# Optimization experiments

Measured on AMD Instinct MI355X. Metric: run time of the kernel, lower is better.

The kernel has to match this reference:

```python
import jax, jax.numpy as jnp
import numpy as np

NEG_SLOPE = 0.2
EPS = 1e-16


def gat_conv(x, edge_index, W, att_src, att_dst, bias, heads, out_ch, concat):
    """PyG-style GATConv (eval mode, add_self_loops=True)."""
    N = x.shape[0]
    h = (x @ W).reshape(N, heads, out_ch)              # [N,H,C]
    loop = jnp.arange(N, dtype=edge_index.dtype)
    src = jnp.concatenate([edge_index[0], loop])       # [E+N]
    dst = jnp.concatenate([edge_index[1], loop])
    a_src = jnp.sum(h * att_src, axis=-1)              # [N,H]
    a_dst = jnp.sum(h * att_dst, axis=-1)
    e = jax.nn.leaky_relu(a_src[src] + a_dst[dst], NEG_SLOPE)  # [E+N,H]
    # segment softmax over destination nodes
    m = jax.ops.segment_max(e, dst, num_segments=N)
    e = jnp.exp(e - m[dst])
    s = jax.ops.segment_sum(e, dst, num_segments=N)
    alpha = e / (s[dst] + EPS)                         # [E+N,H]
    msg = h[src] * alpha[..., None]                    # [E+N,H,C]
    out = jax.ops.segment_sum(msg, dst, num_segments=N)  # [N,H,C]
    out = out.reshape(N, heads * out_ch) if concat else out.mean(axis=1)
    return out + bias


def setup_inputs() -> dict:
    key = jax.random.key(0)
    ks = jax.random.split(key, 11)
    N, F, E = 100000, 128, 1600000
    H1, C1 = 4, 16
    H2, C2 = 1, 16
    return {
        "x": jax.random.normal(ks[0], (N, F), dtype=jnp.float32),
        "edge_index": jax.random.randint(ks[1], (2, E), 0, N, dtype=jnp.int64) if jax.config.jax_enable_x64 else jax.random.randint(ks[1], (2, E), 0, N).astype(jnp.int32),
        "W1": jax.random.normal(ks[2], (F, H1 * C1), dtype=jnp.float32) * 0.1,
        "att_src1": jax.random.normal(ks[3], (H1, C1), dtype=jnp.float32) * 0.1,
        "att_dst1": jax.random.normal(ks[4], (H1, C1), dtype=jnp.float32) * 0.1,
        "bias1": jax.random.normal(ks[5], (H1 * C1,), dtype=jnp.float32) * 0.1,
        "W2": jax.random.normal(ks[6], (H1 * C1, H2 * C2), dtype=jnp.float32) * 0.1,
        "att_src2": jax.random.normal(ks[7], (H2, C2), dtype=jnp.float32) * 0.1,
        "att_dst2": jax.random.normal(ks[8], (H2, C2), dtype=jnp.float32) * 0.1,
        "bias2": jax.random.normal(ks[9], (C2,), dtype=jnp.float32) * 0.1,
    }


def reference(x, edge_index, W1, att_src1, att_dst1, bias1, W2, att_src2, att_dst2, bias2):
    # dropout is identity in eval mode
    h = gat_conv(x, edge_index, W1, att_src1, att_dst1, bias1, heads=4, out_ch=16, concat=True)
    h = jax.nn.elu(h)
    h = gat_conv(h, edge_index, W2, att_src2, att_dst2, bias2, heads=1, out_ch=16, concat=False)
    return jax.nn.log_softmax(h, axis=1)
```

## Files before the change

### kernel.cpp

```cpp
#include <hip/hip_runtime.h>
#include <hip/hip_fp16.h>
#include <hip/hip_bf16.h>
#include <math.h>


#define LRELU(v) ((v) > 0.f ? (v) : 0.2f * (v))
#define BSH 8
#define BCAP 5120
#define CHK 8192
#define CAP1 64
#define CAP2 64

typedef __attribute__((ext_vector_type(8))) short short8;
typedef __attribute__((ext_vector_type(8))) _Float16 half8;
typedef __attribute__((ext_vector_type(4))) float float4v;

static __device__ __forceinline__ short f2bf(float f) {
    __hip_bfloat16 b = __float2bfloat16(f);
    return *reinterpret_cast<short*>(&b);
}

__global__ __launch_bounds__(256) void k_scatter(const int* __restrict__ ei, int* __restrict__ cursor,
                                                 int* __restrict__ stage, int E, int NBK) {
    __shared__ int hist[512];
    __shared__ int cnt2[512];
    __shared__ int base[512];
    int tid = threadIdx.x;
    int e0 = blockIdx.x * CHK;
    int nedge = E - e0; if (nedge > CHK) nedge = CHK;

    for (int i = tid; i < 512; i += 256) { hist[i] = 0; cnt2[i] = 0; }
    __syncthreads();
    for (int j = tid; j < nedge; j += 256) {
        int d = ei[E + e0 + j];
        atomicAdd(&hist[d >> BSH], 1);
    }
    __syncthreads();
    for (int b = tid; b < NBK; b += 256) {
        int c = hist[b];
        if (c > 0) base[b] = b * BCAP + atomicAdd(&cursor[b], c);
    }
    __syncthreads();
    for (int j = tid; j < nedge; j += 256) {
        int s = ei[e0 + j];
        int d = ei[E + e0 + j];
        int b = d >> BSH;
        int r = atomicAdd(&cnt2[b], 1);
        stage[base[b] + r] = s | ((d & ((1 << BSH) - 1)) << 17);
    }
}

__global__ __launch_bounds__(256) void k_build(const int* __restrict__ stage,
                                               const int* __restrict__ cursor,
                                               int* __restrict__ row_start,
                                               int* __restrict__ csr,
                                               const float* __restrict__ W1,
                                               const float* __restrict__ att_src,
                                               const float* __restrict__ att_dst,
                                               float* __restrict__ Wc,
                                               const float* __restrict__ W2,
                                               const float* __restrict__ att_src2,
                                               const float* __restrict__ att_dst2,
                                               float* __restrict__ Wc2,
                                               int NBK, int E, int N) {
    __shared__ int cnt[256];
    __shared__ int lb[256];
    __shared__ int cur[256];
    __shared__ int sA[256];
    int b = blockIdx.x, tid = threadIdx.x;
    int nodes0 = b << BSH;
    int nnodes = N - nodes0; if (nnodes > 256) nnodes = 256;
    int partial = 0;
    for (int i = tid; i < b; i += 256) partial += cursor[i];
    sA[tid] = partial;
    __syncthreads();
    for (int off = 128; off >= 1; off >>= 1) {
        if (tid < off) sA[tid] += sA[tid + off];
        __syncthreads();
    }
    int ebase = sA[0];
    int ecnt = cursor[b];
    __syncthreads();
    if (b == 0) {
        if (tid == 0) row_start[N] = E + N;
        for (int i = tid; i < 16 * 128; i += 256) {
            int col = i >> 7, k = i & 127;
            float v = 0.f;
            if (col < 8) {
                int h = col & 3;
                const float* att = (col < 4) ? att_src : att_dst;
                #pragma unroll
                for (int c = 0; c < 16; c++) v += W1[k * 64 + h * 16 + c] * att[h * 16 + c];
            }
            Wc[i] = v;
        }
        for (int i = tid; i < 128; i += 256) {
            int col = i >> 6, k = i & 63;
            const float* att = col ? att_dst2 : att_src2;
            float v = 0.f;
            #pragma unroll
            for (int c = 0; c < 16; c++) v += W2[k * 16 + c] * att[c];
            Wc2[i] = v;
        }
    }
    const int* sbk = stage + b * BCAP;
    cnt[tid] = (tid < nnodes) ? 1 : 0;
    __syncthreads();
    for (int e = tid; e < ecnt; e += 256) {
        int l = (sbk[e] >> 17) & 255;
        atomicAdd(&cnt[l], 1);
    }
    __syncthreads();
    int myc = cnt[tid];
    sA[tid] = myc;
    __syncthreads();
    for (int off = 1; off < 256; off <<= 1) {
        int r = sA[tid] + ((tid >= off) ? sA[tid - off] : 0);
        __syncthreads();
        sA[tid] = r;
        __syncthreads();
    }
    int gb = ebase + nodes0;
    lb[tid] = sA[tid] - myc;
    cur[tid] = 1;
    __syncthreads();
    if (tid < nnodes) {
        row_start[nodes0 + tid] = gb + lb[tid];
        csr[gb + lb[tid]] = nodes0 + tid;
    }
    __syncthreads();
    for (int e = tid; e < ecnt; e += 256) {
        int v = sbk[e];
        int l = (v >> 17) & 255;
        int src = v & 0x1FFFF;
        int r = atomicAdd(&cur[l], 1);
        csr[gb + lb[l] + r] = src;
    }
}

__global__ __launch_bounds__(256) void k_gemm1(const float* __restrict__ x,
                                               const float* __restrict__ W1,
                                               const float* __restrict__ Wc,
                                               __half* __restrict__ h1, float* __restrict__ a_src,
                                               float* __restrict__ a_dst, int N) {
    __shared__ short wt[80 * 136];
    int tid = threadIdx.x;
    for (int i = tid; i < 128 * 64; i += 256) {
        int k = i >> 6, c = i & 63;
        wt[c * 136 + k] = f2bf(W1[i]);
    }
    for (int i = tid; i < 16 * 128; i += 256) {
        int col = i >> 7, k = i & 127;
        wt[(64 + col) * 136 + k] = f2bf(Wc[i]);
    }
    __syncthreads();
    int wave = tid >> 6, lane = tid & 63;
    int m = lane & 15, q = lane >> 4;
    int nbase = blockIdx.x * 64 + wave * 16;
    int anode = nbase + m;
    bool rowok = anode < N;
    const float* xrow = x + (size_t)(rowok ? anode : 0) * 128 + q * 8;

    float4v acc[5];
    #pragma unroll
    for (int ct = 0; ct < 5; ct++)
        #pragma unroll
        for (int r = 0; r < 4; r++) acc[ct][r] = 0.f;

    #pragma unroll
    for (int kc = 0; kc < 4; kc++) {
        float4 u0 = make_float4(0.f, 0.f, 0.f, 0.f), u1 = u0;
        if (rowok) {
            u0 = *(const float4*)(xrow + kc * 32);
            u1 = *(const float4*)(xrow + kc * 32 + 4);
        }
        short8 af;
        af[0] = f2bf(u0.x); af[1] = f2bf(u0.y); af[2] = f2bf(u0.z); af[3] = f2bf(u0.w);
        af[4] = f2bf(u1.x); af[5] = f2bf(u1.y); af[6] = f2bf(u1.z); af[7] = f2bf(u1.w);
        #pragma unroll
        for (int ct = 0; ct < 5; ct++) {
            short8 bf = *(const short8*)&wt[(ct * 16 + m) * 136 + kc * 32 + q * 8];
            acc[ct] = __builtin_amdgcn_mfma_f32_16x16x32_bf16(af, bf, acc[ct], 0, 0, 0);
        }
    }
    #pragma unroll
    for (int ct = 0; ct < 4; ct++) {
        #pragma unroll
        for (int r = 0; r < 4; r++) {
            int n = nbase + q * 4 + r;
            if (n < N) h1[(size_t)n * 64 + ct * 16 + m] = __float2half(acc[ct][r]);
        }
    }
    #pragma unroll
    for (int r = 0; r < 4; r++) {
        int n = nbase + q * 4 + r;
        if (n < N) {
            float v = acc[4][r];
            if (m < 4) a_src[n * 4 + m] = v;
            else if (m < 8) a_dst[n * 4 + (m - 4)] = v;
        }
    }
}

__global__ __launch_bounds__(256) void k_agg1(const int* __restrict__ row_start,
                                              const int* __restrict__ csr_src,
                                              const float* __restrict__ a_src,
                                              const float* __restrict__ a_dst,
                                              const __half* __restrict__ h1,
                                              const float* __restrict__ bias,
                                              __half* __restrict__ out1, int N) {
    __shared__ int   sidx[16][CAP1];
    __shared__ float sval[16][CAP1 * 4];
    int tid = threadIdx.x;
    int wave = tid >> 6, lane = tid & 63;
    int quad = lane >> 4, l16 = lane & 15;
    int slot = wave * 4 + quad;
    int node = blockIdx.x * 16 + slot;
    if (node >= N) return;
    int row = row_start[node];
    int deg = row_start[node + 1] - row;
    float4 ad = ((const float4*)a_dst)[node];
    float s0 = 0.f, s1 = 0.f, s2 = 0.f, s3 = 0.f;
    for (int j = l16; j < deg; j += 16) {
        int s = csr_src[row + j];
        float4 as = ((const float4*)a_src)[s];
        float e0 = __expf(LRELU(as.x + ad.x));
        float e1 = __expf(LRELU(as.y + ad.y));
        float e2 = __expf(LRELU(as.z + ad.z));
        float e3 = __expf(LRELU(as.w + ad.w));
        if (j < CAP1) {
            sidx[slot][j] = s;
            *(float4*)&sval[slot][j * 4] = make_float4(e0, e1, e2, e3);
        }
        s0 += e0; s1 += e1; s2 += e2; s3 += e3;
    }
    #pragma unroll
    for (int m = 1; m < 16; m <<= 1) {
        s0 += __shfl_xor(s0, m, 64);
        s1 += __shfl_xor(s1, m, 64);
        s2 += __shfl_xor(s2, m, 64);
        s3 += __shfl_xor(s3, m, 64);
    }
    int myh = l16 >> 2;
    float ssv = myh == 0 ? s0 : myh == 1 ? s1 : myh == 2 ? s2 : s3;
    float adm = myh == 0 ? ad.x : myh == 1 ? ad.y : myh == 2 ? ad.z : ad.w;
    float iv = 1.f / (ssv + 1e-16f);
    float A0 = 0.f, A1 = 0.f, A2 = 0.f, A3 = 0.f;
    float B0 = 0.f, B1 = 0.f, B2 = 0.f, B3 = 0.f;
    int dc = deg < CAP1 ? deg : CAP1;
    int j = 0;
    for (; j + 8 <= dc; j += 8) {
        int t[8]; float e[8]; float2 lo[8], hi[8];
        #pragma unroll
        for (int u = 0; u < 8; u++) {
            t[u] = sidx[slot][j + u];
            e[u] = sval[slot][(j + u) * 4 + myh];
        }
        #pragma unroll
        for (int u = 0; u < 8; u++) {
            union { float2 f; __half2 h[2]; } uu;
            uu.f = *(const float2*)&h1[(size_t)t[u] * 64 + l16 * 4];
            lo[u] = __half22float2(uu.h[0]);
            hi[u] = __half22float2(uu.h[1]);
        }
        #pragma unroll
        for (int u = 0; u < 8; u += 2) {
            A0 += e[u] * lo[u].x; A1 += e[u] * lo[u].y;
            A2 += e[u] * hi[u].x; A3 += e[u] * hi[u].y;
            B0 += e[u + 1] * lo[u + 1].x; B1 += e[u + 1] * lo[u + 1].y;
            B2 += e[u + 1] * hi[u + 1].x; B3 += e[u + 1] * hi[u + 1].y;
        }
    }
    for (; j < dc; j++) {
        int t = sidx[slot][j];
        float e = sval[slot][j * 4 + myh];
        union { float2 f; __half2 h[2]; } uu;
        uu.f = *(const float2*)&h1[(size_t)t * 64 + l16 * 4];
        float2 lo = __half22float2(uu.h[0]), hi = __half22float2(uu.h[1]);
        A0 += e * lo.x; A1 += e * lo.y; A2 += e * hi.x; A3 += e * hi.y;
    }
    for (; j < deg; j++) {
        int s = csr_src[row + j];
        float e = __expf(LRELU(a_src[s * 4 + myh] + adm));
        union { float2 f; __half2 h[2]; } uu;
        uu.f = *(const float2*)&h1[(size_t)s * 64 + l16 * 4];
        float2 lo = __half22float2(uu.h[0]), hi = __half22float2(uu.h[1]);
        A0 += e * lo.x; A1 += e * lo.y; A2 += e * hi.x; A3 += e * hi.y;
    }
    A0 += B0; A1 += B1; A2 += B2; A3 += B3;
    float4 bb = ((const float4*)bias)[l16];
    float o0 = A0 * iv + bb.x;
    float o1 = A1 * iv + bb.y;
    float o2 = A2 * iv + bb.z;
    float o3 = A3 * iv + bb.w;
    o0 = (o0 > 0.f) ? o0 : (__expf(o0) - 1.f);
    o1 = (o1 > 0.f) ? o1 : (__expf(o1) - 1.f);
    o2 = (o2 > 0.f) ? o2 : (__expf(o2) - 1.f);
    o3 = (o3 > 0.f) ? o3 : (__expf(o3) - 1.f);
    union { __half2 h2v[2]; float2 f2; } pk;
    pk.h2v[0] = __floats2half2_rn(o0, o1);
    pk.h2v[1] = __floats2half2_rn(o2, o3);
    *(float2*)&out1[(size_t)node * 64 + l16 * 4] = pk.f2;
}

__global__ __launch_bounds__(256) void k_gemm2(const __half* __restrict__ out1,
                                               const float* __restrict__ W2,
                                               const float* __restrict__ Wc2,
                                               __half* __restrict__ h2, float* __restrict__ a_src,
                                               float* __restrict__ a_dst, int N) {
    __shared__ _Float16 wt2[16][72];
    __shared__ _Float16 wtb[16][72];
    int tid = threadIdx.x;
    for (int i = tid; i < 16 * 64; i += 256) {
        int k = i >> 4, c = i & 15;
        wt2[c][k] = (_Float16)W2[i];
    }
    for (int i = tid; i < 16 * 64; i += 256) {
        int col = i >> 6, k = i & 63;
        wtb[col][k] = (col < 2) ? (_Float16)Wc2[col * 64 + k] : (_Float16)0.f;
    }
    __syncthreads();
    int wave = tid >> 6, lane = tid & 63;
    int m = lane & 15, q = lane >> 4;
    int nbase = blockIdx.x * 64 + wave * 16;
    int anode = nbase + m;
    bool ok = anode < N;
    const __half* arow = out1 + (size_t)(ok ? anode : 0) * 64 + q * 8;

    float4v c1 = {0.f, 0.f, 0.f, 0.f}, c2v = {0.f, 0.f, 0.f, 0.f};
    #pragma unroll
    for (int kc = 0; kc < 2; kc++) {
        half8 af = *(const half8*)(arow + kc * 32);
        half8 b1 = *(const half8*)&wt2[m][kc * 32 + q * 8];
        half8 b2 = *(const half8*)&wtb[m][kc * 32 + q * 8];
        c1  = __builtin_amdgcn_mfma_f32_16x16x32_f16(af, b1, c1, 0, 0, 0);
        c2v = __builtin_amdgcn_mfma_f32_16x16x32_f16(af, b2, c2v, 0, 0, 0);
    }
    #pragma unroll
    for (int r = 0; r < 4; r++) {
        int n = nbase + q * 4 + r;
        if (n < N) {
            h2[(size_t)n * 16 + m] = __float2half(c1[r]);
            if (m == 0) a_src[n] = c2v[r];
            else if (m == 1) a_dst[n] = c2v[r];
        }
    }
}

__global__ __launch_bounds__(256) void k_agg2(const int* __restrict__ row_start,
                                              const int* __restrict__ csr_src,
                                              const float* __restrict__ a_src,
                                              const float* __restrict__ a_dst,
                                              const __half* __restrict__ h2,
                                              const float* __restrict__ bias,
                                              float* __restrict__ out, int N) {
    __shared__ int   sidx[16][CAP2];
    __shared__ float sval[16][CAP2];
    int tid = threadIdx.x;
    int wave = tid >> 6, lane = tid & 63;
    int quad = lane >> 4, l16 = lane & 15;
    int slot = wave * 4 + quad;
    int node = blockIdx.x * 16 + slot;
    if (node >= N) return;
    int row = row_start[node];
    int deg = row_start[node + 1] - row;
    float ad = a_dst[node];
    float sh = 0.f;
    for (int j = l16; j < deg; j += 16) {
        int s = csr_src[row + j];
        float e = __expf(LRELU(a_src[s] + ad));
        if (j < CAP2) { sidx[slot][j] = s; sval[slot][j] = e; }
        sh += e;
    }
    #pragma unroll
    for (int m = 1; m < 16; m <<= 1) sh += __shfl_xor(sh, m, 64);
    float iv = 1.f / (sh + 1e-16f);
    int cg = l16 & 7, eg = l16 >> 3;
    float ax = 0.f, ay = 0.f, bx = 0.f, by = 0.f;
    int dc = deg < CAP2 ? deg : CAP2;
    int j = eg;
    for (; j + 6 < dc; j += 8) {
        int t0 = sidx[slot][j], t1 = sidx[slot][j + 2];
        int t2 = sidx[slot][j + 4], t3 = sidx[slot][j + 6];
        float e0 = sval[slot][j], e1 = sval[slot][j + 2];
        float e2 = sval[slot][j + 4], e3 = sval[slot][j + 6];
        float2 g0 = __half22float2(*(const __half2*)&h2[(size_t)t0 * 16 + cg * 2]);
        float2 g1 = __half22float2(*(const __half2*)&h2[(size_t)t1 * 16 + cg * 2]);
        float2 g2 = __half22float2(*(const __half2*)&h2[(size_t)t2 * 16 + cg * 2]);
        float2 g3 = __half22float2(*(const __half2*)&h2[(size_t)t3 * 16 + cg * 2]);
        ax += e0 * g0.x + e2 * g2.x; ay += e0 * g0.y + e2 * g2.y;
        bx += e1 * g1.x + e3 * g3.x; by += e1 * g1.y + e3 * g3.y;
    }
    for (; j < deg; j += 2) {
        int s; float e;
        if (j < dc) { s = sidx[slot][j]; e = sval[slot][j]; }
        else { s = csr_src[row + j]; e = __expf(LRELU(a_src[s] + ad)); }
        float2 g = __half22float2(*(const __half2*)&h2[(size_t)s * 16 + cg * 2]);
        ax += e * g.x; ay += e * g.y;
    }
    ax += bx; ay += by;
    ax += __shfl_xor(ax, 8, 64);
    ay += __shfl_xor(ay, 8, 64);
    float2 bb = ((const float2*)bias)[cg];
    float vx = ax * iv + bb.x;
    float vy = ay * iv + bb.y;
    float mx = fmaxf(vx, vy);
    #pragma unroll
    for (int m = 1; m < 8; m <<= 1) mx = fmaxf(mx, __shfl_xor(mx, m, 64));
    float se = __expf(vx - mx) + __expf(vy - mx);
    #pragma unroll
    for (int m = 1; m < 8; m <<= 1) se += __shfl_xor(se, m, 64);
    float ls = mx + __logf(se);
    if (eg == 0)
        ((float2*)out)[(size_t)node * 8 + cg] = make_float2(vx - ls, vy - ls);
}

extern "C" void kernel_launch(void* const* d_in, const int* in_sizes, int n_in,
                              void* d_out, int out_size, void* d_ws, size_t ws_size,
                              hipStream_t stream) {
    const float* x        = (const float*)d_in[0];
    const int*   ei       = (const int*)d_in[1];
    const float* W1       = (const float*)d_in[2];
    const float* att_src1 = (const float*)d_in[3];
    const float* att_dst1 = (const float*)d_in[4];
    const float* bias1    = (const float*)d_in[5];
    const float* W2       = (const float*)d_in[6];
    const float* att_src2 = (const float*)d_in[7];
    const float* att_dst2 = (const float*)d_in[8];
    const float* bias2    = (const float*)d_in[9];
    float* out = (float*)d_out;

    const int N = in_sizes[0] / 128;
    const int E = in_sizes[1] / 2;
    const int NBK = (N + 255) >> BSH;

    char* p = (char*)d_ws;
    auto alloc = [&](size_t bytes) -> void* {
        void* r = (void*)p;
        p += (bytes + 255) & ~(size_t)255;
        return r;
    };
    __half* h1     = (__half*)alloc((size_t)N * 64 * 2);
    __half* out1   = (__half*)alloc((size_t)N * 64 * 2);
    __half* h2     = (__half*)alloc((size_t)N * 16 * 2);
    float* a_src1  = (float*)alloc((size_t)N * 4 * 4);
    float* a_dst1  = (float*)alloc((size_t)N * 4 * 4);
    float* a_src2  = (float*)alloc((size_t)N * 4);
    float* a_dst2  = (float*)alloc((size_t)N * 4);
    float* Wc      = (float*)alloc(16 * 128 * 4);
    float* Wc2     = (float*)alloc(2 * 64 * 4);
    int*   row_st  = (int*)alloc((size_t)(N + 1) * 4);
    int*   csr     = (int*)alloc((size_t)(E + N) * 4);
    int*   stage   = (int*)alloc((size_t)NBK * BCAP * 4);
    int*   cursor  = (int*)alloc((size_t)NBK * 4);
    (void)ws_size; (void)n_in; (void)out_size;

    hipMemsetAsync(cursor, 0, (size_t)NBK * 4, stream);
    k_scatter<<<(E + CHK - 1) / CHK, 256, 0, stream>>>(ei, cursor, stage, E, NBK);
    k_build<<<NBK, 256, 0, stream>>>(stage, cursor, row_st, csr,
                                     W1, att_src1, att_dst1, Wc,
                                     W2, att_src2, att_dst2, Wc2, NBK, E, N);
    k_gemm1<<<(N + 63) / 64, 256, 0, stream>>>(x, W1, Wc, h1, a_src1, a_dst1, N);
    k_agg1<<<(N + 15) / 16, 256, 0, stream>>>(row_st, csr, a_src1, a_dst1, h1, bias1, out1, N);
    k_gemm2<<<(N + 63) / 64, 256, 0, stream>>>(out1, W2, Wc2, h2, a_src2, a_dst2, N);
    k_agg2<<<(N + 15) / 16, 256, 0, stream>>>(row_st, csr, a_src2, a_dst2, h2, bias2, out, N);
}
```

Before: 234.5 us.

## Remap aggregation kernels to four lanes per node with single-pass softmax

Both aggregation kernels now give each destination node 4 lanes (one per head in layer 1, one column quarter in layer 2) instead of 16. The two-phase scheme with LDS staging of edge indices and exp values is replaced by a single pass that accumulates the unnormalised weighted sum and the softmax denominator together, with wider 16-byte feature gathers. This removes shared memory, the cross-lane reductions and the second pass over edges, but each lane carries more registers and works through the degree loop serially, which may reduce memory-level parallelism per node.

```diff
diff --git a/kernel.cpp b/kernel.cpp
--- a/kernel.cpp
+++ b/kernel.cpp
@@ -8,11 +8,10 @@
 #define BSH 8
 #define BCAP 5120
 #define CHK 8192
-#define CAP1 64
-#define CAP2 64
 
 typedef __attribute__((ext_vector_type(8))) short short8;
 typedef __attribute__((ext_vector_type(8))) _Float16 half8;
+typedef __attribute__((ext_vector_type(4))) _Float16 half4;
 typedef __attribute__((ext_vector_type(4))) float float4v;
 
 static __device__ __forceinline__ short f2bf(float f) {
@@ -209,98 +208,82 @@
                                               const __half* __restrict__ h1,
                                               const float* __restrict__ bias,
                                               __half* __restrict__ out1, int N) {
-    __shared__ int   sidx[16][CAP1];
-    __shared__ float sval[16][CAP1 * 4];
     int tid = threadIdx.x;
     int wave = tid >> 6, lane = tid & 63;
-    int quad = lane >> 4, l16 = lane & 15;
-    int slot = wave * 4 + quad;
-    int node = blockIdx.x * 16 + slot;
+    int grp = lane >> 2, sub = lane & 3;
+    int node = blockIdx.x * 64 + wave * 16 + grp;
     if (node >= N) return;
     int row = row_start[node];
     int deg = row_start[node + 1] - row;
-    float4 ad = ((const float4*)a_dst)[node];
-    float s0 = 0.f, s1 = 0.f, s2 = 0.f, s3 = 0.f;
-    for (int j = l16; j < deg; j += 16) {
-        int s = csr_src[row + j];
-        float4 as = ((const float4*)a_src)[s];
-        float e0 = __expf(LRELU(as.x + ad.x));
-        float e1 = __expf(LRELU(as.y + ad.y));
-        float e2 = __expf(LRELU(as.z + ad.z));
-        float e3 = __expf(LRELU(as.w + ad.w));
-        if (j < CAP1) {
-            sidx[slot][j] = s;
-            *(float4*)&sval[slot][j * 4] = make_float4(e0, e1, e2, e3);
-        }
-        s0 += e0; s1 += e1; s2 += e2; s3 += e3;
-    }
-    #pragma unroll
-    for (int m = 1; m < 16; m <<= 1) {
-        s0 += __shfl_xor(s0, m, 64);
-        s1 += __shfl_xor(s1, m, 64);
-        s2 += __shfl_xor(s2, m, 64);
-        s3 += __shfl_xor(s3, m, 64);
-    }
-    int myh = l16 >> 2;
-    float ssv = myh == 0 ? s0 : myh == 1 ? s1 : myh == 2 ? s2 : s3;
-    float adm = myh == 0 ? ad.x : myh == 1 ? ad.y : myh == 2 ? ad.z : ad.w;
-    float iv = 1.f / (ssv + 1e-16f);
-    float A0 = 0.f, A1 = 0.f, A2 = 0.f, A3 = 0.f;
-    float B0 = 0.f, B1 = 0.f, B2 = 0.f, B3 = 0.f;
-    int dc = deg < CAP1 ? deg : CAP1;
+    float adm = a_dst[node * 4 + sub];
+    const _Float16* hb = (const _Float16*)h1 + sub * 16;
+    float A[16];
+    #pragma unroll
+    for (int c = 0; c < 16; c++) A[c] = 0.f;
+    float sh = 0.f;
     int j = 0;
-    for (; j + 8 <= dc; j += 8) {
-        int t[8]; float e[8]; float2 lo[8], hi[8];
+    for (; j + 4 <= deg; j += 4) {
+        int s0 = csr_src[row + j + 0];
+        int s1 = csr_src[row + j + 1];
+        int s2 = csr_src[row + j + 2];
+        int s3 = csr_src[row + j + 3];
+        float x0 = a_src[s0 * 4 + sub] + adm;
+        float x1 = a_src[s1 * 4 + sub] + adm;
+        float x2 = a_src[s2 * 4 + sub] + adm;
+        float x3 = a_src[s3 * 4 + sub] + adm;
+        half8 p0 = *(const half8*)(hb + (size_t)s0 * 64);
+        half8 q0 = *(const half8*)(hb + (size_t)s0 * 64 + 8);
+        half8 p1 = *(const half8*)(hb + (size_t)s1 * 64);
+        half8 q1 = *(const half8*)(hb + (size_t)s1 * 64 + 8);
+        half8 p2 = *(const half8*)(hb + (size_t)s2 * 64);
+        half8 q2 = *(const half8*)(hb + (size_t)s2 * 64 + 8);
+        half8 p3 = *(const half8*)(hb + (size_t)s3 * 64);
+        half8 q3 = *(const half8*)(hb + (size_t)s3 * 64 + 8);
+        float e0 = __expf(fmaxf(x0, 0.2f * x0));
+        float e1 = __expf(fmaxf(x1, 0.2f * x1));
+        float e2 = __expf(fmaxf(x2, 0.2f * x2));
+        float e3 = __expf(fmaxf(x3, 0.2f * x3));
+        sh += (e0 + e1) + (e2 + e3);
         #pragma unroll
-        for (int u = 0; u < 8; u++) {
-            t[u] = sidx[slot][j + u];
-            e[u] = sval[slot][(j + u) * 4 + myh];
-        }
-        #pragma unroll
-        for (int u = 0; u < 8; u++) {
-            union { float2 f; __half2 h[2]; } uu;
-            uu.f = *(const float2*)&h1[(size_t)t[u] * 64 + l16 * 4];
-            lo[u] = __half22float2(uu.h[0]);
-            hi[u] = __half22float2(uu.h[1]);
-        }
-        #pragma unroll
-        for (int u = 0; u < 8; u += 2) {
-            A0 += e[u] * lo[u].x; A1 += e[u] * lo[u].y;
-            A2 += e[u] * hi[u].x; A3 += e[u] * hi[u].y;
-            B0 += e[u + 1] * lo[u + 1].x; B1 += e[u + 1] * lo[u + 1].y;
-            B2 += e[u + 1] * hi[u + 1].x; B3 += e[u + 1] * hi[u + 1].y;
-        }
-    }
-    for (; j < dc; j++) {
-        int t = sidx[slot][j];
-        float e = sval[slot][j * 4 + myh];
-        union { float2 f; __half2 h[2]; } uu;
-        uu.f = *(const float2*)&h1[(size_t)t * 64 + l16 * 4];
-        float2 lo = __half22float2(uu.h[0]), hi = __half22float2(uu.h[1]);
-        A0 += e * lo.x; A1 += e * lo.y; A2 += e * hi.x; A3 += e * hi.y;
+        for (int c = 0; c < 8; c++) {
+            A[c]     += e0 * (float)p0[c] + e1 * (float)p1[c]
+                      + e2 * (float)p2[c] + e3 * (float)p3[c];
+            A[c + 8] += e0 * (float)q0[c] + e1 * (float)q1[c]
+                      + e2 * (float)q2[c] + e3 * (float)q3[c];
+        }
     }
     for (; j < deg; j++) {
         int s = csr_src[row + j];
-        float e = __expf(LRELU(a_src[s * 4 + myh] + adm));
-        union { float2 f; __half2 h[2]; } uu;
-        uu.f = *(const float2*)&h1[(size_t)s * 64 + l16 * 4];
-        float2 lo = __half22float2(uu.h[0]), hi = __half22float2(uu.h[1]);
-        A0 += e * lo.x; A1 += e * lo.y; A2 += e * hi.x; A3 += e * hi.y;
-    }
-    A0 += B0; A1 += B1; A2 += B2; A3 += B3;
-    float4 bb = ((const float4*)bias)[l16];
-    float o0 = A0 * iv + bb.x;
-    float o1 = A1 * iv + bb.y;
-    float o2 = A2 * iv + bb.z;
-    float o3 = A3 * iv + bb.w;
-    o0 = (o0 > 0.f) ? o0 : (__expf(o0) - 1.f);
-    o1 = (o1 > 0.f) ? o1 : (__expf(o1) - 1.f);
-    o2 = (o2 > 0.f) ? o2 : (__expf(o2) - 1.f);
-    o3 = (o3 > 0.f) ? o3 : (__expf(o3) - 1.f);
-    union { __half2 h2v[2]; float2 f2; } pk;
-    pk.h2v[0] = __floats2half2_rn(o0, o1);
-    pk.h2v[1] = __floats2half2_rn(o2, o3);
-    *(float2*)&out1[(size_t)node * 64 + l16 * 4] = pk.f2;
+        float xv = a_src[s * 4 + sub] + adm;
+        half8 p = *(const half8*)(hb + (size_t)s * 64);
+        half8 q = *(const half8*)(hb + (size_t)s * 64 + 8);
+        float e = __expf(fmaxf(xv, 0.2f * xv));
+        sh += e;
+        #pragma unroll
+        for (int c = 0; c < 8; c++) {
+            A[c]     += e * (float)p[c];
+            A[c + 8] += e * (float)q[c];
+        }
+    }
+    float iv = 1.f / (sh + 1e-16f);
+    const float4* bb = (const float4*)bias + sub * 4;
+    union { __half2 h2v[8]; float4 f4[2]; } pk;
+    #pragma unroll
+    for (int c4 = 0; c4 < 4; c4++) {
+        float4 b = bb[c4];
+        float o0 = A[c4 * 4 + 0] * iv + b.x;
+        float o1 = A[c4 * 4 + 1] * iv + b.y;
+        float o2 = A[c4 * 4 + 2] * iv + b.z;
+        float o3 = A[c4 * 4 + 3] * iv + b.w;
+        o0 = (o0 > 0.f) ? o0 : (__expf(o0) - 1.f);
+        o1 = (o1 > 0.f) ? o1 : (__expf(o1) - 1.f);
+        o2 = (o2 > 0.f) ? o2 : (__expf(o2) - 1.f);
+        o3 = (o3 > 0.f) ? o3 : (__expf(o3) - 1.f);
+        pk.h2v[c4 * 2 + 0] = __floats2half2_rn(o0, o1);
+        pk.h2v[c4 * 2 + 1] = __floats2half2_rn(o2, o3);
+    }
+    *(float4*)&out1[(size_t)node * 64 + sub * 16]     = pk.f4[0];
+    *(float4*)&out1[(size_t)node * 64 + sub * 16 + 8] = pk.f4[1];
 }
 
 __global__ __launch_bounds__(256) void k_gemm2(const __half* __restrict__ out1,
@@ -354,65 +337,67 @@
                                               const __half* __restrict__ h2,
                                               const float* __restrict__ bias,
                                               float* __restrict__ out, int N) {
-    __shared__ int   sidx[16][CAP2];
-    __shared__ float sval[16][CAP2];
     int tid = threadIdx.x;
     int wave = tid >> 6, lane = tid & 63;
-    int quad = lane >> 4, l16 = lane & 15;
-    int slot = wave * 4 + quad;
-    int node = blockIdx.x * 16 + slot;
+    int grp = lane >> 2, sub = lane & 3;
+    int node = blockIdx.x * 64 + wave * 16 + grp;
     if (node >= N) return;
     int row = row_start[node];
     int deg = row_start[node + 1] - row;
     float ad = a_dst[node];
+    const _Float16* hb = (const _Float16*)h2 + sub * 4;
+    float A0 = 0.f, A1 = 0.f, A2 = 0.f, A3 = 0.f;
     float sh = 0.f;
-    for (int j = l16; j < deg; j += 16) {
+    int j = 0;
+    for (; j + 4 <= deg; j += 4) {
+        int s0 = csr_src[row + j + 0];
+        int s1 = csr_src[row + j + 1];
+        int s2 = csr_src[row + j + 2];
+        int s3 = csr_src[row + j + 3];
+        float x0 = a_src[s0] + ad;
+        float x1 = a_src[s1] + ad;
+        float x2 = a_src[s2] + ad;
+        float x3 = a_src[s3] + ad;
+        half4 v0 = *(const half4*)(hb + (size_t)s0 * 16);
+        half4 v1 = *(const half4*)(hb + (size_t)s1 * 16);
+        half4 v2 = *(const half4*)(hb + (size_t)s2 * 16);
+        half4 v3 = *(const half4*)(hb + (size_t)s3 * 16);
+        float e0 = __expf(fmaxf(x0, 0.2f * x0));
+        float e1 = __expf(fmaxf(x1, 0.2f * x1));
+        float e2 = __expf(fmaxf(x2, 0.2f * x2));
+        float e3 = __expf(fmaxf(x3, 0.2f * x3));
+        sh += (e0 + e1) + (e2 + e3);
+        A0 += e0 * (float)v0[0] + e1 * (float)v1[0] + e2 * (float)v2[0] + e3 * (float)v3[0];
+        A1 += e0 * (float)v0[1] + e1 * (float)v1[1] + e2 * (float)v2[1] + e3 * (float)v3[1];
+        A2 += e0 * (float)v0[2] + e1 * (float)v1[2] + e2 * (float)v2[2] + e3 * (float)v3[2];
+        A3 += e0 * (float)v0[3] + e1 * (float)v1[3] + e2 * (float)v2[3] + e3 * (float)v3[3];
+    }
+    for (; j < deg; j++) {
         int s = csr_src[row + j];
-        float e = __expf(LRELU(a_src[s] + ad));
-        if (j < CAP2) { sidx[slot][j] = s; sval[slot][j] = e; }
+        float xv = a_src[s] + ad;
+        half4 v = *(const half4*)(hb + (size_t)s * 16);
+        float e = __expf(fmaxf(xv, 0.2f * xv));
         sh += e;
-    }
-    #pragma unroll
-    for (int m = 1; m < 16; m <<= 1) sh += __shfl_xor(sh, m, 64);
+        A0 += e * (float)v[0];
+        A1 += e * (float)v[1];
+        A2 += e * (float)v[2];
+        A3 += e * (float)v[3];
+    }
     float iv = 1.f / (sh + 1e-16f);
-    int cg = l16 & 7, eg = l16 >> 3;
-    float ax = 0.f, ay = 0.f, bx = 0.f, by = 0.f;
-    int dc = deg < CAP2 ? deg : CAP2;
-    int j = eg;
-    for (; j + 6 < dc; j += 8) {
-        int t0 = sidx[slot][j], t1 = sidx[slot][j + 2];
-        int t2 = sidx[slot][j + 4], t3 = sidx[slot][j + 6];
-        float e0 = sval[slot][j], e1 = sval[slot][j + 2];
-        float e2 = sval[slot][j + 4], e3 = sval[slot][j + 6];
-        float2 g0 = __half22float2(*(const __half2*)&h2[(size_t)t0 * 16 + cg * 2]);
-        float2 g1 = __half22float2(*(const __half2*)&h2[(size_t)t1 * 16 + cg * 2]);
-        float2 g2 = __half22float2(*(const __half2*)&h2[(size_t)t2 * 16 + cg * 2]);
-        float2 g3 = __half22float2(*(const __half2*)&h2[(size_t)t3 * 16 + cg * 2]);
-        ax += e0 * g0.x + e2 * g2.x; ay += e0 * g0.y + e2 * g2.y;
-        bx += e1 * g1.x + e3 * g3.x; by += e1 * g1.y + e3 * g3.y;
-    }
-    for (; j < deg; j += 2) {
-        int s; float e;
-        if (j < dc) { s = sidx[slot][j]; e = sval[slot][j]; }
-        else { s = csr_src[row + j]; e = __expf(LRELU(a_src[s] + ad)); }
-        float2 g = __half22float2(*(const __half2*)&h2[(size_t)s * 16 + cg * 2]);
-        ax += e * g.x; ay += e * g.y;
-    }
-    ax += bx; ay += by;
-    ax += __shfl_xor(ax, 8, 64);
-    ay += __shfl_xor(ay, 8, 64);
-    float2 bb = ((const float2*)bias)[cg];
-    float vx = ax * iv + bb.x;
-    float vy = ay * iv + bb.y;
-    float mx = fmaxf(vx, vy);
-    #pragma unroll
-    for (int m = 1; m < 8; m <<= 1) mx = fmaxf(mx, __shfl_xor(mx, m, 64));
-    float se = __expf(vx - mx) + __expf(vy - mx);
-    #pragma unroll
-    for (int m = 1; m < 8; m <<= 1) se += __shfl_xor(se, m, 64);
+    float4 b = ((const float4*)bias)[sub];
+    float v0 = A0 * iv + b.x;
+    float v1 = A1 * iv + b.y;
+    float v2 = A2 * iv + b.z;
+    float v3 = A3 * iv + b.w;
+    float mx = fmaxf(fmaxf(v0, v1), fmaxf(v2, v3));
+    mx = fmaxf(mx, __shfl_xor(mx, 1, 64));
+    mx = fmaxf(mx, __shfl_xor(mx, 2, 64));
+    float se = __expf(v0 - mx) + __expf(v1 - mx) + __expf(v2 - mx) + __expf(v3 - mx);
+    se += __shfl_xor(se, 1, 64);
+    se += __shfl_xor(se, 2, 64);
     float ls = mx + __logf(se);
-    if (eg == 0)
-        ((float2*)out)[(size_t)node * 8 + cg] = make_float2(vx - ls, vy - ls);
+    *(float4*)&out[(size_t)node * 16 + sub * 4] =
+        make_float4(v0 - ls, v1 - ls, v2 - ls, v3 - ls);
 }
 
 extern "C" void kernel_launch(void* const* d_in, const int* in_sizes, int n_in,
@@ -461,7 +446,7 @@
                                      W1, att_src1, att_dst1, Wc,
                                      W2, att_src2, att_dst2, Wc2, NBK, E, N);
     k_gemm1<<<(N + 63) / 64, 256, 0, stream>>>(x, W1, Wc, h1, a_src1, a_dst1, N);
-    k_agg1<<<(N + 15) / 16, 256, 0, stream>>>(row_st, csr, a_src1, a_dst1, h1, bias1, out1, N);
+    k_agg1<<<(N + 63) / 64, 256, 0, stream>>>(row_st, csr, a_src1, a_dst1, h1, bias1, out1, N);
     k_gemm2<<<(N + 63) / 64, 256, 0, stream>>>(out1, W2, Wc2, h2, a_src2, a_dst2, N);
-    k_agg2<<<(N + 15) / 16, 256, 0, stream>>>(row_st, csr, a_src2, a_dst2, h2, bias2, out, N);
-}
+    k_agg2<<<(N + 63) / 64, 256, 0, stream>>>(row_st, csr, a_src2, a_dst2, h2, bias2, out, N);
+}
```

Measured after the change: 236.6 us. No clear change (+0.9%).
